# Kernel tuning notes

Measured on AMD Instinct MI355X. Metric: run time of the kernel, lower is better.

## Reference

```python
import jax, jax.numpy as jnp
import numpy as np

N_HEADS = 16


def setup_inputs() -> dict:
    key = jax.random.key(0)
    ks = jax.random.split(key, 9)
    B, S, D = 4, 2048, 1024
    query = jax.random.normal(ks[0], (B, S, D), dtype=jnp.float32)
    key_t = jax.random.normal(ks[1], (B, S, D), dtype=jnp.float32)
    value = jax.random.normal(ks[2], (B, S, D), dtype=jnp.float32)
    mask = jax.random.randint(ks[3], (B, 1, S, S), 0, 10) > 0
    scale_w = 0.02  # keep exp(attention) in a safe range
    Wq = jax.random.normal(ks[4], (D, D), dtype=jnp.float32) * scale_w
    Wk = jax.random.normal(ks[5], (D, D), dtype=jnp.float32) * scale_w
    Wv = jax.random.normal(ks[6], (D, D), dtype=jnp.float32) * scale_w
    fc_w = jax.random.normal(ks[7], (D, D), dtype=jnp.float32) * scale_w
    fc_b = jnp.zeros((D,), dtype=jnp.float32)
    return {"query": query, "key": key_t, "value": value, "mask": mask,
            "Wq": Wq, "Wk": Wk, "Wv": Wv, "fc_w": fc_w, "fc_b": fc_b}


def reference(query, key, value, mask, Wq, Wk, Wv, fc_w, fc_b):
    B, S, D = query.shape
    H = N_HEADS
    Dh = D // H
    scale = jnp.sqrt(jnp.asarray(D / H, dtype=query.dtype))
    # Faithful to original: direct reshape [B,S,D] -> [B,H,S,Dh] (no transpose)
    Q = (query @ Wq.T).reshape(B, H, S, Dh)
    K = (key @ Wk.T).reshape(B, H, S, Dh)
    V = (value @ Wv.T).reshape(B, H, S, Dh)
    attn = jnp.einsum('bhqd,bhkd->bhqk', Q, K) / scale  # [B,H,S,S]
    # Hand-rolled masked softmax: exp, masked_fill(False->0), normalize, nan->0
    temp = jnp.where(mask, jnp.exp(attn), 0.0)
    attn = temp / jnp.sum(temp, axis=-1, keepdims=True)
    attn = jnp.where(jnp.isnan(attn), 0.0, attn)
    res = jnp.einsum('bhqk,bhkd->bhqd', attn, V)  # [B,H,S,Dh]
    outs = res.transpose(0, 2, 1, 3).reshape(B, S, D)
    outs = outs @ fc_w.T + fc_b
    return outs, res.transpose(1, 0, 2, 3)
```

## Files before the change

kernel.cpp:

```cpp
#include <hip/hip_runtime.h>


typedef __attribute__((ext_vector_type(8))) short bf16x8;
typedef __attribute__((ext_vector_type(4))) short bf16x4;
typedef __attribute__((ext_vector_type(4))) float f32x4;

#define MFMA32(a, b, c) __builtin_amdgcn_mfma_f32_16x16x32_bf16(a, b, c, 0, 0, 0)

static __device__ __forceinline__ float fast_exp2(float x) {
#if __has_builtin(__builtin_amdgcn_exp2f)
  return __builtin_amdgcn_exp2f(x);
#else
  return __expf(x * 0.69314718056f);
#endif
}

__device__ __forceinline__ unsigned short fbf(float f) {
  union { float f; unsigned u; } x; x.f = f;
  unsigned r = x.u + 0x7fffu + ((x.u >> 16) & 1u);
  return (unsigned short)(r >> 16);
}

static __device__ __forceinline__ bf16x4 pack2(unsigned lo, unsigned hi) {
  union { unsigned u[2]; bf16x4 v; } x; x.u[0] = lo; x.u[1] = hi; return x.v;
}

static __device__ __forceinline__ bf16x8 cat2(bf16x4 lo, bf16x4 hi) {
  union { bf16x4 h[2]; bf16x8 v; } x; x.h[0] = lo; x.h[1] = hi; return x.v;
}

static __device__ __forceinline__ bf16x4 epp(f32x4 s, unsigned pre, int sh) {
  union { float f; unsigned u; } e0, e1, e2, e3;
  e0.f = fast_exp2(s[0]); e1.f = fast_exp2(s[1]);
  e2.f = fast_exp2(s[2]); e3.f = fast_exp2(s[3]);
  unsigned p01 = __builtin_amdgcn_perm(e1.u + 0x8000u, e0.u + 0x8000u, 0x07060302u);
  unsigned p23 = __builtin_amdgcn_perm(e3.u + 0x8000u, e2.u + 0x8000u, 0x07060302u);
  int m0 = __builtin_amdgcn_sbfe(pre, sh + 0, 1), m1 = __builtin_amdgcn_sbfe(pre, sh + 1, 1);
  int m2 = __builtin_amdgcn_sbfe(pre, sh + 2, 1), m3 = __builtin_amdgcn_sbfe(pre, sh + 3, 1);
  unsigned k01 = __builtin_amdgcn_perm((unsigned)m1, (unsigned)m0, 0x07060100u);
  unsigned k23 = __builtin_amdgcn_perm((unsigned)m3, (unsigned)m2, 0x07060100u);
  return pack2(p01 & k01, p23 & k23);
}

__global__ __launch_bounds__(256) void f2b3_kernel(const float* __restrict__ s0,
                                                   const float* __restrict__ s1,
                                                   const float* __restrict__ s2,
                                                   unsigned short* __restrict__ d0,
                                                   unsigned short* __restrict__ d1,
                                                   unsigned short* __restrict__ d2) {
  int z = blockIdx.y;
  const float* s = (z == 0) ? s0 : (z == 1) ? s1 : s2;
  unsigned short* d = (z == 0) ? d0 : (z == 1) ? d1 : d2;
  int i = blockIdx.x * 256 + threadIdx.x;
  float4 v = ((const float4*)s)[i];
  ushort4 o;
  o.x = fbf(v.x); o.y = fbf(v.y); o.z = fbf(v.z); o.w = fbf(v.w);
  ((ushort4*)d)[i] = o;
}

__global__ __launch_bounds__(256) void f2b4_kernel(const float* __restrict__ s0,
                                                   const float* __restrict__ s1,
                                                   const float* __restrict__ s2,
                                                   const float* __restrict__ s3,
                                                   unsigned short* __restrict__ d0,
                                                   unsigned short* __restrict__ d1,
                                                   unsigned short* __restrict__ d2,
                                                   unsigned short* __restrict__ d3) {
  int z = blockIdx.y;
  const float* s = (z == 0) ? s0 : (z == 1) ? s1 : (z == 2) ? s2 : s3;
  unsigned short* d = (z == 0) ? d0 : (z == 1) ? d1 : (z == 2) ? d2 : d3;
  int i = blockIdx.x * 256 + threadIdx.x;
  float4 v = ((const float4*)s)[i];
  ushort4 o;
  o.x = fbf(v.x); o.y = fbf(v.y); o.z = fbf(v.z); o.w = fbf(v.w);
  ((ushort4*)d)[i] = o;
}

__global__ __launch_bounds__(256) void pack_mask_kernel(const int* __restrict__ m,
                                                        unsigned long long* __restrict__ o) {
  int i = blockIdx.x * 256 + threadIdx.x;
  unsigned long long b = __ballot(m[i] != 0);
  if ((threadIdx.x & 63) == 0) {
    int row = i >> 11;
    int kt = (i >> 7) & 15;
    int h = (i >> 6) & 1;
    o[(kt * 8192 + row) * 2 + h] = b;
  }
}

__global__ __launch_bounds__(256) void vtrans_kernel(const unsigned short* __restrict__ Vf,
                                                     unsigned short* __restrict__ Vt) {
  __shared__ unsigned short T[64][72];
  const int bh = blockIdx.y;
  const int s0 = blockIdx.x * 64;
  const int tid = threadIdx.x;
  {
    int r = tid >> 2, c = (tid & 3) * 16;
    const unsigned short* src = Vf + bh * 131072 + (s0 + r) * 64 + c;
    uint4 v0 = *(const uint4*)(src);
    uint4 v1 = *(const uint4*)(src + 8);
    *(uint4*)&T[r][c] = v0;
    *(uint4*)&T[r][c + 8] = v1;
  }
  __syncthreads();
  {
    int dh = tid & 63, rb = (tid >> 6) * 16;
    unsigned short o[16];
#pragma unroll
    for (int j = 0; j < 16; ++j) o[j] = T[rb + j][dh];
    unsigned short* dst = Vt + bh * 131072 + dh * 2048 + s0 + rb;
    *(uint4*)dst = *(const uint4*)&o[0];
    *(uint4*)(dst + 8) = *(const uint4*)&o[8];
  }
}

__global__ __launch_bounds__(256) void proj_kernel(const unsigned short* __restrict__ A0,
                                                   const unsigned short* __restrict__ A1,
                                                   const unsigned short* __restrict__ A2,
                                                   const unsigned short* __restrict__ W0,
                                                   const unsigned short* __restrict__ W1,
                                                   const unsigned short* __restrict__ W2,
                                                   unsigned short* __restrict__ C0,
                                                   unsigned short* __restrict__ C1,
                                                   unsigned short* __restrict__ C2) {
  __shared__ unsigned short Alds[128 * 32];
  __shared__ unsigned short Blds[128 * 32];
  const int flat = (blockIdx.z * 64 + blockIdx.y) * 8 + blockIdx.x;
  const int wid = (flat & 7) * 192 + (flat >> 3);
  const int z = wid >> 9;
  const int by = (wid >> 3) & 63;
  const int bx = wid & 7;
  const unsigned short* A = (z == 0) ? A0 : (z == 1) ? A1 : A2;
  const unsigned short* B = (z == 0) ? W0 : (z == 1) ? W1 : W2;
  const int tid = threadIdx.x;
  const int w = tid >> 6, l = tid & 63, q4 = l >> 4, c16 = l & 15;
  const int wm = w & 1, wn = w >> 1;
  const int mBase = by * 128, nBase = bx * 128;

  f32x4 acc[4][4];
#pragma unroll
  for (int a0 = 0; a0 < 4; ++a0)
#pragma unroll
    for (int a1 = 0; a1 < 4; ++a1) acc[a0][a1] = (f32x4){0.f, 0.f, 0.f, 0.f};

  const int r0 = tid >> 2, cc0 = tid & 3;

  for (int kt = 0; kt < 32; ++kt) {
    __syncthreads();
    const unsigned short* ga0 = A + (mBase + r0) * 1024 + kt * 32 + cc0 * 8;
    const unsigned short* ga1 = A + (mBase + 64 + r0) * 1024 + kt * 32 + cc0 * 8;
    const unsigned short* gb0 = B + (nBase + r0) * 1024 + kt * 32 + cc0 * 8;
    const unsigned short* gb1 = B + (nBase + 64 + r0) * 1024 + kt * 32 + cc0 * 8;
    __builtin_amdgcn_global_load_lds((const __attribute__((address_space(1))) void*)ga0,
                                     (__attribute__((address_space(3))) void*)(&Alds[tid * 8]),
                                     16, 0, 0);
    __builtin_amdgcn_global_load_lds((const __attribute__((address_space(1))) void*)ga1,
                                     (__attribute__((address_space(3))) void*)(&Alds[(tid + 256) * 8]),
                                     16, 0, 0);
    __builtin_amdgcn_global_load_lds((const __attribute__((address_space(1))) void*)gb0,
                                     (__attribute__((address_space(3))) void*)(&Blds[tid * 8]),
                                     16, 0, 0);
    __builtin_amdgcn_global_load_lds((const __attribute__((address_space(1))) void*)gb1,
                                     (__attribute__((address_space(3))) void*)(&Blds[(tid + 256) * 8]),
                                     16, 0, 0);
    __syncthreads();

    bf16x8 af[4], bfr[4];
#pragma unroll
    for (int mi = 0; mi < 4; ++mi)
      af[mi] = *(const bf16x8*)&Alds[(wm * 64 + mi * 16 + c16) * 32 + q4 * 8];
#pragma unroll
    for (int ni = 0; ni < 4; ++ni)
      bfr[ni] = *(const bf16x8*)&Blds[(wn * 64 + ni * 16 + c16) * 32 + q4 * 8];
#pragma unroll
    for (int mi = 0; mi < 4; ++mi)
#pragma unroll
      for (int ni = 0; ni < 4; ++ni) acc[mi][ni] = MFMA32(af[mi], bfr[ni], acc[mi][ni]);
  }

  unsigned short* C = (z == 0) ? C0 : (z == 1) ? C1 : C2;
  const float scale = (z == 0) ? 0.18033688f : 1.0f;
#pragma unroll
  for (int mi = 0; mi < 4; ++mi) {
#pragma unroll
    for (int ni = 0; ni < 4; ++ni) {
#pragma unroll
      for (int rg = 0; rg < 4; ++rg) {
        int row = mBase + wm * 64 + mi * 16 + q4 * 4 + rg;
        int col = nBase + wn * 64 + ni * 16 + c16;
        C[row * 1024 + col] = fbf(acc[mi][ni][rg] * scale);
      }
    }
  }
}

__global__ __launch_bounds__(256) void gemm_out(const unsigned short* __restrict__ A,
                                                const unsigned short* __restrict__ B,
                                                float* __restrict__ C,
                                                const float* __restrict__ bias) {
  __shared__ unsigned short Alds[128 * 32];
  __shared__ unsigned short Blds[128 * 32];
  const int flat = blockIdx.y * 8 + blockIdx.x;
  const int wid = (flat & 7) * 64 + (flat >> 3);
  const int by = wid >> 3, bx = wid & 7;
  const int tid = threadIdx.x;
  const int w = tid >> 6, l = tid & 63, q4 = l >> 4, c16 = l & 15;
  const int wm = w & 1, wn = w >> 1;
  const int mBase = by * 128, nBase = bx * 128;

  f32x4 acc[4][4];
#pragma unroll
  for (int a0 = 0; a0 < 4; ++a0)
#pragma unroll
    for (int a1 = 0; a1 < 4; ++a1) acc[a0][a1] = (f32x4){0.f, 0.f, 0.f, 0.f};

  const int r0 = tid >> 2, cc0 = tid & 3;

  for (int kt = 0; kt < 32; ++kt) {
    __syncthreads();
    const unsigned short* ga0 = A + (mBase + r0) * 1024 + kt * 32 + cc0 * 8;
    const unsigned short* ga1 = A + (mBase + 64 + r0) * 1024 + kt * 32 + cc0 * 8;
    const unsigned short* gb0 = B + (nBase + r0) * 1024 + kt * 32 + cc0 * 8;
    const unsigned short* gb1 = B + (nBase + 64 + r0) * 1024 + kt * 32 + cc0 * 8;
    __builtin_amdgcn_global_load_lds((const __attribute__((address_space(1))) void*)ga0,
                                     (__attribute__((address_space(3))) void*)(&Alds[tid * 8]),
                                     16, 0, 0);
    __builtin_amdgcn_global_load_lds((const __attribute__((address_space(1))) void*)ga1,
                                     (__attribute__((address_space(3))) void*)(&Alds[(tid + 256) * 8]),
                                     16, 0, 0);
    __builtin_amdgcn_global_load_lds((const __attribute__((address_space(1))) void*)gb0,
                                     (__attribute__((address_space(3))) void*)(&Blds[tid * 8]),
                                     16, 0, 0);
    __builtin_amdgcn_global_load_lds((const __attribute__((address_space(1))) void*)gb1,
                                     (__attribute__((address_space(3))) void*)(&Blds[(tid + 256) * 8]),
                                     16, 0, 0);
    __syncthreads();

    bf16x8 af[4], bfr[4];
#pragma unroll
    for (int mi = 0; mi < 4; ++mi)
      af[mi] = *(const bf16x8*)&Alds[(wm * 64 + mi * 16 + c16) * 32 + q4 * 8];
#pragma unroll
    for (int ni = 0; ni < 4; ++ni)
      bfr[ni] = *(const bf16x8*)&Blds[(wn * 64 + ni * 16 + c16) * 32 + q4 * 8];
#pragma unroll
    for (int mi = 0; mi < 4; ++mi)
#pragma unroll
      for (int ni = 0; ni < 4; ++ni) acc[mi][ni] = MFMA32(af[mi], bfr[ni], acc[mi][ni]);
  }

#pragma unroll
  for (int mi = 0; mi < 4; ++mi) {
#pragma unroll
    for (int ni = 0; ni < 4; ++ni) {
#pragma unroll
      for (int rg = 0; rg < 4; ++rg) {
        int row = mBase + wm * 64 + mi * 16 + q4 * 4 + rg;
        int col = nBase + wn * 64 + ni * 16 + c16;
        C[row * 1024 + col] = acc[mi][ni][rg] + bias[col];
      }
    }
  }
}

__global__ __launch_bounds__(256, 4) void flash_kernel(const unsigned short* __restrict__ Q,
                                                       const unsigned short* __restrict__ K,
                                                       const unsigned short* __restrict__ Vt,
                                                       const uint4* __restrict__ mb,
                                                       unsigned short* __restrict__ Cws,
                                                       float* __restrict__ res2) {
  __shared__ unsigned short Klds[128 * 64];
  __shared__ unsigned short Vtlds[64 * 128];
  const int tid = threadIdx.x;
  const int w = tid >> 6, l = tid & 63, q4 = l >> 4, c16 = l & 15;
  const int q44 = q4 * 4;
  const int flat = (blockIdx.z * 16 + blockIdx.y) * 16 + blockIdx.x;
  const int wid = (flat & 7) * 128 + (flat >> 3);
  const int qt = wid & 15, h = (wid >> 4) & 15, b = wid >> 8;
  const unsigned short* Qh = Q + (b * 2048 + h * 128) * 1024;
  const unsigned short* Kh = K + (b * 2048 + h * 128) * 1024;
  const unsigned short* Vth = Vt + (b * 16 + h) * 64 * 2048;

  bf16x8 qf[2][2];
#pragma unroll
  for (int i = 0; i < 2; ++i)
#pragma unroll
    for (int kc = 0; kc < 2; ++kc)
      qf[i][kc] = *(const bf16x8*)(Qh + (qt * 128 + w * 32 + i * 16 + c16) * 64 + kc * 32 + q4 * 8);

  const int rowi = b * 2048 + qt * 128 + w * 32 + c16;

  const int kOff = (tid >> 3) * 64 + (((tid & 7) ^ ((tid >> 3) & 7)) * 8);
  const int vOff = (tid >> 4) * 2048 + (((tid & 15) ^ (tid >> 4)) * 8);

  const int kb0 = c16 * 64 + ((q4 ^ (c16 & 7)) * 8);
  const int kb1 = kb0 ^ 32;
  const int vb = c16 * 128 + (q4 & 1) * 4;
  const int q41 = q4 >> 1;

  const bf16x8 ones8 = {(short)0x3F80, (short)0x3F80, (short)0x3F80, (short)0x3F80,
                        (short)0x3F80, (short)0x3F80, (short)0x3F80, (short)0x3F80};

  f32x4 oacc[2][4], soacc[2];
#pragma unroll
  for (int i = 0; i < 2; ++i) {
    soacc[i] = (f32x4){0.f, 0.f, 0.f, 0.f};
#pragma unroll
    for (int t = 0; t < 4; ++t) oacc[i][t] = (f32x4){0.f, 0.f, 0.f, 0.f};
  }

  for (int kt = 0; kt < 16; ++kt) {
    const unsigned short* gk = Kh + kt * 8192 + kOff;
    const unsigned short* gv = Vth + kt * 128 + vOff;
#pragma unroll
    for (int j = 0; j < 4; ++j) {
      __builtin_amdgcn_global_load_lds((const __attribute__((address_space(1))) void*)(gk + j * 2048),
                                       (__attribute__((address_space(3))) void*)(&Klds[(j * 256 + tid) * 8]),
                                       16, 0, 0);
      __builtin_amdgcn_global_load_lds((const __attribute__((address_space(1))) void*)(gv + j * 32768),
                                       (__attribute__((address_space(3))) void*)(&Vtlds[(j * 256 + tid) * 8]),
                                       16, 0, 0);
    }
    uint4 m0 = mb[kt * 8192 + rowi];
    uint4 m1 = mb[kt * 8192 + rowi + 16];
    unsigned pre0[4] = {m0.x >> q44, m0.y >> q44, m0.z >> q44, m0.w >> q44};
    unsigned pre1[4] = {m1.x >> q44, m1.y >> q44, m1.z >> q44, m1.w >> q44};
    __syncthreads();

#pragma unroll
    for (int m = 0; m < 4; ++m) {
      bf16x8 kfE0 = *(const bf16x8*)(Klds + kb0 + (2 * m) * 1024);
      bf16x8 kfE1 = *(const bf16x8*)(Klds + kb1 + (2 * m) * 1024);
      bf16x8 kfO0 = *(const bf16x8*)(Klds + kb0 + (2 * m + 1) * 1024);
      bf16x8 kfO1 = *(const bf16x8*)(Klds + kb1 + (2 * m + 1) * 1024);
      f32x4 sE0 = {0.f, 0.f, 0.f, 0.f}, sE1 = {0.f, 0.f, 0.f, 0.f};
      f32x4 sO0 = {0.f, 0.f, 0.f, 0.f}, sO1 = {0.f, 0.f, 0.f, 0.f};
      sE0 = MFMA32(kfE0, qf[0][0], sE0); sE0 = MFMA32(kfE1, qf[0][1], sE0);
      sE1 = MFMA32(kfE0, qf[1][0], sE1); sE1 = MFMA32(kfE1, qf[1][1], sE1);
      sO0 = MFMA32(kfO0, qf[0][0], sO0); sO0 = MFMA32(kfO1, qf[0][1], sO0);
      sO1 = MFMA32(kfO0, qf[1][0], sO1); sO1 = MFMA32(kfO1, qf[1][1], sO1);

      int shE = 0, shO = 16;
      bf16x8 pf0 = cat2(epp(sE0, pre0[m], shE), epp(sO0, pre0[m], shO));
      bf16x8 pf1 = cat2(epp(sE1, pre1[m], shE), epp(sO1, pre1[m], shO));

      int pLo = (4 * m + q41) ^ c16;
      int aLo = vb + pLo * 8;
#pragma unroll
      for (int t = 0; t < 4; ++t) {
        bf16x4 vlo = *(const bf16x4*)(Vtlds + aLo + t * 2048);
        bf16x4 vhi = *(const bf16x4*)(Vtlds + (aLo ^ 16) + t * 2048);
        bf16x8 vf8 = cat2(vlo, vhi);
        oacc[0][t] = MFMA32(vf8, pf0, oacc[0][t]);
        oacc[1][t] = MFMA32(vf8, pf1, oacc[1][t]);
      }
      soacc[0] = MFMA32(ones8, pf0, soacc[0]);
      soacc[1] = MFMA32(ones8, pf1, soacc[1]);
    }
    __syncthreads();
  }

#pragma unroll
  for (int i = 0; i < 2; ++i) {
    float sum = soacc[i][0];
    float rcp = (sum > 0.f) ? (1.0f / sum) : 0.f;
    int q = qt * 128 + w * 32 + i * 16 + c16;
    float* rp = res2 + (((h * 4 + b) * 2048 + q) * 64 + q44);
    unsigned short* cp = Cws + ((b * 2048 + q) * 1024 + h * 64 + q44);
#pragma unroll
    for (int t = 0; t < 4; ++t) {
      float o0 = oacc[i][t][0] * rcp, o1 = oacc[i][t][1] * rcp;
      float o2 = oacc[i][t][2] * rcp, o3 = oacc[i][t][3] * rcp;
      float4 fo = {o0, o1, o2, o3};
      *(float4*)(rp + t * 16) = fo;
      ushort4 cv = {fbf(o0), fbf(o1), fbf(o2), fbf(o3)};
      *(ushort4*)(cp + t * 16) = cv;
    }
  }
}

extern "C" void kernel_launch(void* const* d_in, const int* in_sizes, int n_in,
                              void* d_out, int out_size, void* d_ws, size_t ws_size,
                              hipStream_t stream) {
  const float* query = (const float*)d_in[0];
  const float* key_t = (const float*)d_in[1];
  const float* value = (const float*)d_in[2];
  const int* mask = (const int*)d_in[3];
  const float* Wq = (const float*)d_in[4];
  const float* Wk = (const float*)d_in[5];
  const float* Wv = (const float*)d_in[6];
  const float* fcw = (const float*)d_in[7];
  const float* fcb = (const float*)d_in[8];
  float* out = (float*)d_out;

  char* ws = (char*)d_ws;
  unsigned short* qbf = (unsigned short*)(ws);
  unsigned short* kbf = (unsigned short*)(ws + (16u << 20));
  unsigned short* vbf = (unsigned short*)(ws + (32u << 20));
  unsigned short* wqb = (unsigned short*)(ws + (48u << 20));
  unsigned short* wkb = (unsigned short*)(ws + (50u << 20));
  unsigned short* wvb = (unsigned short*)(ws + (52u << 20));
  unsigned short* fwb = (unsigned short*)(ws + (54u << 20));
  unsigned short* Qf = (unsigned short*)(ws + (56u << 20));
  unsigned short* Kf = (unsigned short*)(ws + (72u << 20));
  unsigned short* Vnat = (unsigned short*)(ws + (88u << 20));
  unsigned short* Cws = qbf;
  unsigned long long* mbits = (unsigned long long*)kbf;
  unsigned short* Vt = vbf;

  f2b3_kernel<<<dim3(8192, 3), 256, 0, stream>>>(query, key_t, value, qbf, kbf, vbf);
  f2b4_kernel<<<dim3(1024, 4), 256, 0, stream>>>(Wq, Wk, Wv, fcw, wqb, wkb, wvb, fwb);

  proj_kernel<<<dim3(8, 64, 3), 256, 0, stream>>>(qbf, kbf, vbf, wqb, wkb, wvb, Qf, Kf, Vnat);

  vtrans_kernel<<<dim3(32, 64), 256, 0, stream>>>(Vnat, Vt);

  pack_mask_kernel<<<65536, 256, 0, stream>>>(mask, mbits);

  flash_kernel<<<dim3(16, 16, 4), 256, 0, stream>>>(Qf, Kf, Vt, (const uint4*)mbits, Cws,
                                                    out + 8388608);

  gemm_out<<<dim3(8, 64), 256, 0, stream>>>(Cws, fwb, out, fcb);
}
```

Measured before the change: 408.6 us.

## Fuse fp32-to-bf16 input conversion into projection GEMM and read V directly

Removes the separate f2b3 conversion kernel. The projection GEMM now loads fp32 activations into a swizzled LDS tile and converts them to bf16 with packed cvt instructions before the MFMAs, which avoids a full round trip of the inputs through bf16 workspace. The flash kernel drops its V LDS staging and reads V fragments straight from global memory per lane. The exp-to-bf16 packing now uses the hardware cvt_pk instruction. The costs are twice the LDS bytes for the A tile, and uncoalesced global V loads inside the inner loop that may stall the attention kernel.

```diff
diff --git a/kernel.cpp b/kernel.cpp
--- a/kernel.cpp
+++ b/kernel.cpp
@@ -29,33 +29,26 @@
   union { bf16x4 h[2]; bf16x8 v; } x; x.h[0] = lo; x.h[1] = hi; return x.v;
 }
 
+static __device__ __forceinline__ bf16x8 cvt8(f32x4 a, f32x4 b) {
+  union { unsigned u[4]; bf16x8 v; } x;
+  asm("v_cvt_pk_bf16_f32 %0, %1, %2" : "=v"(x.u[0]) : "v"(a[0]), "v"(a[1]));
+  asm("v_cvt_pk_bf16_f32 %0, %1, %2" : "=v"(x.u[1]) : "v"(a[2]), "v"(a[3]));
+  asm("v_cvt_pk_bf16_f32 %0, %1, %2" : "=v"(x.u[2]) : "v"(b[0]), "v"(b[1]));
+  asm("v_cvt_pk_bf16_f32 %0, %1, %2" : "=v"(x.u[3]) : "v"(b[2]), "v"(b[3]));
+  return x.v;
+}
+
 static __device__ __forceinline__ bf16x4 epp(f32x4 s, unsigned pre, int sh) {
-  union { float f; unsigned u; } e0, e1, e2, e3;
-  e0.f = fast_exp2(s[0]); e1.f = fast_exp2(s[1]);
-  e2.f = fast_exp2(s[2]); e3.f = fast_exp2(s[3]);
-  unsigned p01 = __builtin_amdgcn_perm(e1.u + 0x8000u, e0.u + 0x8000u, 0x07060302u);
-  unsigned p23 = __builtin_amdgcn_perm(e3.u + 0x8000u, e2.u + 0x8000u, 0x07060302u);
+  float e0 = fast_exp2(s[0]), e1 = fast_exp2(s[1]);
+  float e2 = fast_exp2(s[2]), e3 = fast_exp2(s[3]);
+  unsigned p01, p23;
+  asm("v_cvt_pk_bf16_f32 %0, %1, %2" : "=v"(p01) : "v"(e0), "v"(e1));
+  asm("v_cvt_pk_bf16_f32 %0, %1, %2" : "=v"(p23) : "v"(e2), "v"(e3));
   int m0 = __builtin_amdgcn_sbfe(pre, sh + 0, 1), m1 = __builtin_amdgcn_sbfe(pre, sh + 1, 1);
   int m2 = __builtin_amdgcn_sbfe(pre, sh + 2, 1), m3 = __builtin_amdgcn_sbfe(pre, sh + 3, 1);
   unsigned k01 = __builtin_amdgcn_perm((unsigned)m1, (unsigned)m0, 0x07060100u);
   unsigned k23 = __builtin_amdgcn_perm((unsigned)m3, (unsigned)m2, 0x07060100u);
   return pack2(p01 & k01, p23 & k23);
-}
-
-__global__ __launch_bounds__(256) void f2b3_kernel(const float* __restrict__ s0,
-                                                   const float* __restrict__ s1,
-                                                   const float* __restrict__ s2,
-                                                   unsigned short* __restrict__ d0,
-                                                   unsigned short* __restrict__ d1,
-                                                   unsigned short* __restrict__ d2) {
-  int z = blockIdx.y;
-  const float* s = (z == 0) ? s0 : (z == 1) ? s1 : s2;
-  unsigned short* d = (z == 0) ? d0 : (z == 1) ? d1 : d2;
-  int i = blockIdx.x * 256 + threadIdx.x;
-  float4 v = ((const float4*)s)[i];
-  ushort4 o;
-  o.x = fbf(v.x); o.y = fbf(v.y); o.z = fbf(v.z); o.w = fbf(v.w);
-  ((ushort4*)d)[i] = o;
 }
 
 __global__ __launch_bounds__(256) void f2b4_kernel(const float* __restrict__ s0,
@@ -114,23 +107,23 @@
   }
 }
 
-__global__ __launch_bounds__(256) void proj_kernel(const unsigned short* __restrict__ A0,
-                                                   const unsigned short* __restrict__ A1,
-                                                   const unsigned short* __restrict__ A2,
+__global__ __launch_bounds__(256) void proj_kernel(const float* __restrict__ A0,
+                                                   const float* __restrict__ A1,
+                                                   const float* __restrict__ A2,
                                                    const unsigned short* __restrict__ W0,
                                                    const unsigned short* __restrict__ W1,
                                                    const unsigned short* __restrict__ W2,
                                                    unsigned short* __restrict__ C0,
                                                    unsigned short* __restrict__ C1,
                                                    unsigned short* __restrict__ C2) {
-  __shared__ unsigned short Alds[128 * 32];
+  __shared__ float Af[128 * 32];
   __shared__ unsigned short Blds[128 * 32];
   const int flat = (blockIdx.z * 64 + blockIdx.y) * 8 + blockIdx.x;
   const int wid = (flat & 7) * 192 + (flat >> 3);
   const int z = wid >> 9;
   const int by = (wid >> 3) & 63;
   const int bx = wid & 7;
-  const unsigned short* A = (z == 0) ? A0 : (z == 1) ? A1 : A2;
+  const float* A = (z == 0) ? A0 : (z == 1) ? A1 : A2;
   const unsigned short* B = (z == 0) ? W0 : (z == 1) ? W1 : W2;
   const int tid = threadIdx.x;
   const int w = tid >> 6, l = tid & 63, q4 = l >> 4, c16 = l & 15;
@@ -144,19 +137,19 @@
     for (int a1 = 0; a1 < 4; ++a1) acc[a0][a1] = (f32x4){0.f, 0.f, 0.f, 0.f};
 
   const int r0 = tid >> 2, cc0 = tid & 3;
+  const int ar = tid >> 3, aw = (tid & 7) ^ ((tid >> 3) & 7);
 
   for (int kt = 0; kt < 32; ++kt) {
     __syncthreads();
-    const unsigned short* ga0 = A + (mBase + r0) * 1024 + kt * 32 + cc0 * 8;
-    const unsigned short* ga1 = A + (mBase + 64 + r0) * 1024 + kt * 32 + cc0 * 8;
+#pragma unroll
+    for (int j = 0; j < 4; ++j) {
+      const float* ga = A + (mBase + j * 32 + ar) * 1024 + kt * 32 + aw * 4;
+      __builtin_amdgcn_global_load_lds((const __attribute__((address_space(1))) void*)ga,
+                                       (__attribute__((address_space(3))) void*)(&Af[j * 1024 + tid * 4]),
+                                       16, 0, 0);
+    }
     const unsigned short* gb0 = B + (nBase + r0) * 1024 + kt * 32 + cc0 * 8;
     const unsigned short* gb1 = B + (nBase + 64 + r0) * 1024 + kt * 32 + cc0 * 8;
-    __builtin_amdgcn_global_load_lds((const __attribute__((address_space(1))) void*)ga0,
-                                     (__attribute__((address_space(3))) void*)(&Alds[tid * 8]),
-                                     16, 0, 0);
-    __builtin_amdgcn_global_load_lds((const __attribute__((address_space(1))) void*)ga1,
-                                     (__attribute__((address_space(3))) void*)(&Alds[(tid + 256) * 8]),
-                                     16, 0, 0);
     __builtin_amdgcn_global_load_lds((const __attribute__((address_space(1))) void*)gb0,
                                      (__attribute__((address_space(3))) void*)(&Blds[tid * 8]),
                                      16, 0, 0);
@@ -167,8 +160,12 @@
 
     bf16x8 af[4], bfr[4];
 #pragma unroll
-    for (int mi = 0; mi < 4; ++mi)
-      af[mi] = *(const bf16x8*)&Alds[(wm * 64 + mi * 16 + c16) * 32 + q4 * 8];
+    for (int mi = 0; mi < 4; ++mi) {
+      int row = wm * 64 + mi * 16 + c16;
+      f32x4 fa0 = *(const f32x4*)&Af[row * 32 + (((2 * q4) ^ (row & 7)) * 4)];
+      f32x4 fa1 = *(const f32x4*)&Af[row * 32 + (((2 * q4 + 1) ^ (row & 7)) * 4)];
+      af[mi] = cvt8(fa0, fa1);
+    }
 #pragma unroll
     for (int ni = 0; ni < 4; ++ni)
       bfr[ni] = *(const bf16x8*)&Blds[(wn * 64 + ni * 16 + c16) * 32 + q4 * 8];
@@ -270,7 +267,6 @@
                                                        unsigned short* __restrict__ Cws,
                                                        float* __restrict__ res2) {
   __shared__ unsigned short Klds[128 * 64];
-  __shared__ unsigned short Vtlds[64 * 128];
   const int tid = threadIdx.x;
   const int w = tid >> 6, l = tid & 63, q4 = l >> 4, c16 = l & 15;
   const int q44 = q4 * 4;
@@ -291,12 +287,10 @@
   const int rowi = b * 2048 + qt * 128 + w * 32 + c16;
 
   const int kOff = (tid >> 3) * 64 + (((tid & 7) ^ ((tid >> 3) & 7)) * 8);
-  const int vOff = (tid >> 4) * 2048 + (((tid & 15) ^ (tid >> 4)) * 8);
 
   const int kb0 = c16 * 64 + ((q4 ^ (c16 & 7)) * 8);
   const int kb1 = kb0 ^ 32;
-  const int vb = c16 * 128 + (q4 & 1) * 4;
-  const int q41 = q4 >> 1;
+  const unsigned short* gvlane = Vth + c16 * 2048 + q44;
 
   const bf16x8 ones8 = {(short)0x3F80, (short)0x3F80, (short)0x3F80, (short)0x3F80,
                         (short)0x3F80, (short)0x3F80, (short)0x3F80, (short)0x3F80};
@@ -311,24 +305,30 @@
 
   for (int kt = 0; kt < 16; ++kt) {
     const unsigned short* gk = Kh + kt * 8192 + kOff;
-    const unsigned short* gv = Vth + kt * 128 + vOff;
 #pragma unroll
     for (int j = 0; j < 4; ++j) {
       __builtin_amdgcn_global_load_lds((const __attribute__((address_space(1))) void*)(gk + j * 2048),
                                        (__attribute__((address_space(3))) void*)(&Klds[(j * 256 + tid) * 8]),
                                        16, 0, 0);
-      __builtin_amdgcn_global_load_lds((const __attribute__((address_space(1))) void*)(gv + j * 32768),
-                                       (__attribute__((address_space(3))) void*)(&Vtlds[(j * 256 + tid) * 8]),
-                                       16, 0, 0);
     }
     uint4 m0 = mb[kt * 8192 + rowi];
     uint4 m1 = mb[kt * 8192 + rowi + 16];
     unsigned pre0[4] = {m0.x >> q44, m0.y >> q44, m0.z >> q44, m0.w >> q44};
     unsigned pre1[4] = {m1.x >> q44, m1.y >> q44, m1.z >> q44, m1.w >> q44};
+    const unsigned short* gvk = gvlane + kt * 128;
     __syncthreads();
 
 #pragma unroll
     for (int m = 0; m < 4; ++m) {
+      const unsigned short* gvm = gvk + 32 * m;
+      bf16x8 vf[4];
+#pragma unroll
+      for (int t = 0; t < 4; ++t) {
+        bf16x4 vlo = *(const bf16x4*)(gvm + t * 32768);
+        bf16x4 vhi = *(const bf16x4*)(gvm + t * 32768 + 16);
+        vf[t] = cat2(vlo, vhi);
+      }
+
       bf16x8 kfE0 = *(const bf16x8*)(Klds + kb0 + (2 * m) * 1024);
       bf16x8 kfE1 = *(const bf16x8*)(Klds + kb1 + (2 * m) * 1024);
       bf16x8 kfO0 = *(const bf16x8*)(Klds + kb0 + (2 * m + 1) * 1024);
@@ -344,15 +344,10 @@
       bf16x8 pf0 = cat2(epp(sE0, pre0[m], shE), epp(sO0, pre0[m], shO));
       bf16x8 pf1 = cat2(epp(sE1, pre1[m], shE), epp(sO1, pre1[m], shO));
 
-      int pLo = (4 * m + q41) ^ c16;
-      int aLo = vb + pLo * 8;
 #pragma unroll
       for (int t = 0; t < 4; ++t) {
-        bf16x4 vlo = *(const bf16x4*)(Vtlds + aLo + t * 2048);
-        bf16x4 vhi = *(const bf16x4*)(Vtlds + (aLo ^ 16) + t * 2048);
-        bf16x8 vf8 = cat2(vlo, vhi);
-        oacc[0][t] = MFMA32(vf8, pf0, oacc[0][t]);
-        oacc[1][t] = MFMA32(vf8, pf1, oacc[1][t]);
+        oacc[0][t] = MFMA32(vf[t], pf0, oacc[0][t]);
+        oacc[1][t] = MFMA32(vf[t], pf1, oacc[1][t]);
       }
       soacc[0] = MFMA32(ones8, pf0, soacc[0]);
       soacc[1] = MFMA32(ones8, pf1, soacc[1]);
@@ -394,9 +389,9 @@
   float* out = (float*)d_out;
 
   char* ws = (char*)d_ws;
-  unsigned short* qbf = (unsigned short*)(ws);
-  unsigned short* kbf = (unsigned short*)(ws + (16u << 20));
-  unsigned short* vbf = (unsigned short*)(ws + (32u << 20));
+  unsigned short* Cws = (unsigned short*)(ws);
+  unsigned long long* mbits = (unsigned long long*)(ws + (16u << 20));
+  unsigned short* Vt = (unsigned short*)(ws + (32u << 20));
   unsigned short* wqb = (unsigned short*)(ws + (48u << 20));
   unsigned short* wkb = (unsigned short*)(ws + (50u << 20));
   unsigned short* wvb = (unsigned short*)(ws + (52u << 20));
@@ -404,14 +399,11 @@
   unsigned short* Qf = (unsigned short*)(ws + (56u << 20));
   unsigned short* Kf = (unsigned short*)(ws + (72u << 20));
   unsigned short* Vnat = (unsigned short*)(ws + (88u << 20));
-  unsigned short* Cws = qbf;
-  unsigned long long* mbits = (unsigned long long*)kbf;
-  unsigned short* Vt = vbf;
-
-  f2b3_kernel<<<dim3(8192, 3), 256, 0, stream>>>(query, key_t, value, qbf, kbf, vbf);
+
   f2b4_kernel<<<dim3(1024, 4), 256, 0, stream>>>(Wq, Wk, Wv, fcw, wqb, wkb, wvb, fwb);
 
-  proj_kernel<<<dim3(8, 64, 3), 256, 0, stream>>>(qbf, kbf, vbf, wqb, wkb, wvb, Qf, Kf, Vnat);
+  proj_kernel<<<dim3(8, 64, 3), 256, 0, stream>>>(query, key_t, value, wqb, wkb, wvb,
+                                                  Qf, Kf, Vnat);
 
   vtrans_kernel<<<dim3(32, 64), 256, 0, stream>>>(Vnat, Vt);
 
```

New measurement: 585.5 us. 43.3% more time.
